# Kernel optimization log

Hardware: AMD Instinct MI355X
Metric: run time of the kernel (lower is better)

## Reference

```python
import jax, jax.numpy as jnp
import numpy as np
from jax import lax

B, T, F_IN = 8, 512, 229
C1 = 48            # model_size_conv // 16
C3 = 96            # model_size_conv // 8
D_CONV = 768       # model_size_conv
D_LSTM = 768       # model_size_lstm
N_PITCH = 88       # MAX_MIDI - MIN_MIDI + 1
N_STATE = 5
EMB = 2
LSTM_IN = D_CONV + N_PITCH * EMB   # 944
FC_IN = C3 * (F_IN // 4)           # 96 * 57 = 5472
BN_EPS = 1e-5


def setup_inputs() -> dict:
    key = jax.random.key(0)
    ks = iter(jax.random.split(key, 64))
    nrm = lambda shape, s=0.05: jax.random.normal(next(ks), shape, jnp.float32) * s
    uni = lambda shape: jax.random.uniform(next(ks), shape, jnp.float32, 0.5, 1.5)
    inp = {
        'mel': jax.random.normal(next(ks), (B, T, F_IN), jnp.float32),
        'conv1_w': nrm((C1, 1, 3, 3)), 'conv1_b': nrm((C1,)),
        'bn1_g': uni((C1,)), 'bn1_b': nrm((C1,)), 'bn1_m': nrm((C1,), 0.1), 'bn1_v': uni((C1,)),
        'conv2_w': nrm((C1, C1, 3, 3)), 'conv2_b': nrm((C1,)),
        'bn2_g': uni((C1,)), 'bn2_b': nrm((C1,)), 'bn2_m': nrm((C1,), 0.1), 'bn2_v': uni((C1,)),
        'conv3_w': nrm((C3, C1, 3, 3)), 'conv3_b': nrm((C3,)),
        'bn3_g': uni((C3,)), 'bn3_b': nrm((C3,)), 'bn3_m': nrm((C3,), 0.1), 'bn3_v': uni((C3,)),
        'fc_w': nrm((D_CONV, FC_IN)), 'fc_b': nrm((D_CONV,)),
        'wih1': nrm((4 * D_LSTM, LSTM_IN)), 'whh1': nrm((4 * D_LSTM, D_LSTM)),
        'bih1': nrm((4 * D_LSTM,)), 'bhh1': nrm((4 * D_LSTM,)),
        'wih2': nrm((4 * D_LSTM, D_LSTM)), 'whh2': nrm((4 * D_LSTM, D_LSTM)),
        'bih2': nrm((4 * D_LSTM,)), 'bhh2': nrm((4 * D_LSTM,)),
        'post_w': nrm((N_PITCH * N_STATE, D_LSTM)), 'post_b': nrm((N_PITCH * N_STATE,)),
        'emb_w': nrm((N_STATE, EMB), 1.0),
    }
    return inp


def _conv_bn_relu(x, w, b, g, be, m, v):
    # x: NCHW, w: OIHW, padding 'SAME' == padding=1 for 3x3
    y = lax.conv_general_dilated(x, w, (1, 1), 'SAME', dimension_numbers=('NCHW', 'OIHW', 'NCHW'))
    y = y + b[None, :, None, None]
    scale = (g / jnp.sqrt(v + BN_EPS))[None, :, None, None]
    y = (y - m[None, :, None, None]) * scale + be[None, :, None, None]
    return jax.nn.relu(y)


def _maxpool12(x):
    # MaxPool2d((1,2)) on NCHW, floor mode
    return lax.reduce_window(x, -jnp.inf, lax.max, (1, 1, 1, 2), (1, 1, 1, 2), 'VALID')


def _lstm_cell(x, h, c, wih, whh, bih, bhh):
    z = x @ wih.T + h @ whh.T + bih + bhh
    i, f, g, o = jnp.split(z, 4, axis=-1)
    c = jax.nn.sigmoid(f) * c + jax.nn.sigmoid(i) * jnp.tanh(g)
    h = jax.nn.sigmoid(o) * jnp.tanh(c)
    return h, c


def _forward(mel, conv1_w, conv1_b, bn1_g, bn1_b, bn1_m, bn1_v,
             conv2_w, conv2_b, bn2_g, bn2_b, bn2_m, bn2_v,
             conv3_w, conv3_b, bn3_g, bn3_b, bn3_m, bn3_v,
             fc_w, fc_b, wih1, whh1, bih1, bhh1, wih2, whh2, bih2, bhh2,
             post_w, post_b, emb_w):
    b = mel.shape[0]
    # --- ConvStack acoustic model (eval mode: dropout = identity) ---
    x = mel[:, None]                                  # (B,1,T,F)
    x = _conv_bn_relu(x, conv1_w, conv1_b, bn1_g, bn1_b, bn1_m, bn1_v)
    x = _conv_bn_relu(x, conv2_w, conv2_b, bn2_g, bn2_b, bn2_m, bn2_v)
    x = _maxpool12(x)
    x = _conv_bn_relu(x, conv3_w, conv3_b, bn3_g, bn3_b, bn3_m, bn3_v)
    x = _maxpool12(x)                                 # (B,C3,T,F//4)
    x = x.transpose(0, 2, 1, 3).reshape(b, -1, FC_IN) # (B,T,C3*F//4)
    acoustic = x @ fc_w.T + fc_b                      # (B,T,768)

    def step(carry, a_t):
        h1, c1, h2, c2, prev = carry                  # prev: (B,88) int32
        emb = emb_w[prev].reshape(prev.shape[0], N_PITCH * EMB)
        xt = jnp.concatenate([a_t, emb], axis=-1)     # (B,944)
        h1n, c1n = _lstm_cell(xt, h1, c1, wih1, whh1, bih1, bhh1)
        h2n, c2n = _lstm_cell(h1n, h2, c2, wih2, whh2, bih2, bhh2)
        logits = (h2n @ post_w.T + post_b).reshape(-1, N_PITCH, N_STATE)
        nprev = jnp.argmax(logits, axis=-1).astype(jnp.int32)  # argmax(softmax)==argmax(logits)
        return (h1n, c1n, h2n, c2n, nprev), logits

    z = jnp.zeros((b, D_LSTM), mel.dtype)
    prev0 = jnp.zeros((b, N_PITCH), jnp.int32)
    _, logits = lax.scan(step, (z, z, z, z, prev0), acoustic.transpose(1, 0, 2))
    return logits.transpose(1, 0, 2, 3)               # (B,T,88,N_STATE)


def reference(mel, conv1_w, conv1_b, bn1_g, bn1_b, bn1_m, bn1_v,
              conv2_w, conv2_b, bn2_g, bn2_b, bn2_m, bn2_v,
              conv3_w, conv3_b, bn3_g, bn3_b, bn3_m, bn3_v,
              fc_w, fc_b, wih1, whh1, bih1, bhh1, wih2, whh2, bih2, bhh2,
              post_w, post_b, emb_w):
    return _forward(mel, conv1_w, conv1_b, bn1_g, bn1_b, bn1_m, bn1_v,
                    conv2_w, conv2_b, bn2_g, bn2_b, bn2_m, bn2_v,
                    conv3_w, conv3_b, bn3_g, bn3_b, bn3_m, bn3_v,
                    fc_w, fc_b, wih1, whh1, bih1, bhh1, wih2, whh2, bih2, bhh2,
                    post_w, post_b, emb_w)
```

## Files before the change

### kernel.cpp

```cpp
#include <hip/hip_runtime.h>
#include <math.h>

#define WS_C3   0u
#define WS_C2CH 22413312u
#define WS_AC   28104192u
#define WS_A1   0u
#define WS_ST   31249920u

__device__ __forceinline__ float sigm(float x){ return 1.0f / (1.0f + expf(-x)); }

__device__ __forceinline__ void cstore(float* p, float v){
  union { float f; unsigned u; } c; c.f = v;
  __hip_atomic_store((unsigned*)p, c.u, __ATOMIC_RELAXED,
                     __HIP_MEMORY_SCOPE_SYSTEM);
}
__device__ __forceinline__ void cload64(const float* p, float& a, float& b){
  unsigned long long u = __hip_atomic_load((const unsigned long long*)p,
                          __ATOMIC_RELAXED, __HIP_MEMORY_SCOPE_SYSTEM);
  union { unsigned long long u; float f[2]; } c; c.u = u;
  a = c.f[0]; b = c.f[1];
}
__device__ __forceinline__ unsigned cloadu(const unsigned* p){
  return __hip_atomic_load(p, __ATOMIC_RELAXED, __HIP_MEMORY_SCOPE_SYSTEM);
}

#define SLOT 16
#define FLG  4112
__device__ __forceinline__ void gbar(unsigned* sy, unsigned bar, int wg){
  __syncthreads();
  const int tid = threadIdx.x;
  if (tid == 0)
    __hip_atomic_store(&sy[SLOT + wg*16], bar, __ATOMIC_RELAXED,
                       __HIP_MEMORY_SCOPE_SYSTEM);
  if (wg == 255){
    if (tid < 64){
      for (;;){
        unsigned m0 = cloadu(&sy[SLOT + (4*tid + 0)*16]);
        unsigned m1 = cloadu(&sy[SLOT + (4*tid + 1)*16]);
        unsigned m2 = cloadu(&sy[SLOT + (4*tid + 2)*16]);
        unsigned m3 = cloadu(&sy[SLOT + (4*tid + 3)*16]);
        unsigned a = m0 < m1 ? m0 : m1;
        unsigned b = m2 < m3 ? m2 : m3;
        unsigned mn = a < b ? a : b;
        if (__all(mn >= bar)) break;
        __builtin_amdgcn_s_sleep(1);
      }
    }
    __syncthreads();
    __hip_atomic_store(&sy[FLG + tid*16], bar, __ATOMIC_RELAXED,
                       __HIP_MEMORY_SCOPE_SYSTEM);
  } else {
    if (tid == 0){
      while (cloadu(&sy[FLG + wg*16]) < bar)
        __builtin_amdgcn_s_sleep(1);
    }
  }
  __syncthreads();
}

__global__ __launch_bounds__(256) void conv2f_k(
    const float* __restrict__ mel, const float* __restrict__ w1,
    const float* __restrict__ b1, const float* __restrict__ g1,
    const float* __restrict__ be1, const float* __restrict__ m1,
    const float* __restrict__ v1,
    const float* __restrict__ w2, const float* __restrict__ b2,
    const float* __restrict__ g2, const float* __restrict__ be2,
    const float* __restrict__ m2, const float* __restrict__ v2,
    float* __restrict__ c2ch, int t0)
{
  __shared__ float act[3*8*240];
  __shared__ float w2s[48*8*12];
  __shared__ float mel5[5*240];
  __shared__ float w1s[48*12];
  __shared__ float sc1[48], sh1[48], sc2[48], sh2[48];
  int tid = threadIdx.x;
  int b = blockIdx.x / 130, lt = blockIdx.x - b*130;
  int t = t0 - 1 + lt;

  int fg = tid % 29, ocg = tid / 29;
  int f0 = fg * 8, oc0 = ocg * 6;

  if (t < 0 || t > 511){
    if (tid < 232){
      for (int o = 0; o < 6; ++o)
        for (int jj = 0; jj < 4; ++jj){
          int fp = fg*4 + jj;
          if (fp < 114)
            c2ch[((b*48 + oc0 + o)*130 + lt)*114 + fp] = 0.f;
        }
    }
    return;
  }

  for (int idx = tid; idx < 5*240; idx += 256){
    int rr = idx / 240, w = idx - rr*240;
    int tt = t + rr - 2, f = w - 2;
    mel5[idx] = (tt >= 0 && tt < 512 && f >= 0 && f < 229)
                ? mel[(b*512 + tt)*229 + f] : 0.f;
  }
  for (int idx = tid; idx < 48*12; idx += 256){
    int c = idx / 12, q = idx - c*12;
    int kh = q >> 2, kw = q & 3;
    w1s[idx] = (kw < 3) ? w1[c*9 + kh*3 + kw] : 0.f;
  }
  if (tid < 48){
    float s1 = g1[tid] / sqrtf(v1[tid] + 1e-5f);
    sc1[tid] = s1; sh1[tid] = be1[tid] + (b1[tid] - m1[tid]) * s1;
    float s2 = g2[tid] / sqrtf(v2[tid] + 1e-5f);
    sc2[tid] = s2; sh2[tid] = be2[tid] + (b2[tid] - m2[tid]) * s2;
  }

  float acc[6][8];
  #pragma unroll
  for (int o = 0; o < 6; ++o)
    #pragma unroll
    for (int j = 0; j < 8; ++j) acc[o][j] = 0.f;

  for (int ch = 0; ch < 6; ++ch){
    int ci0 = ch * 8;
    __syncthreads();
    for (int idx = tid; idx < 3*8*240; idx += 256){
      int rr = idx / 1920;
      int rem = idx - rr*1920;
      int ci = rem / 240, w = rem - ci*240;
      int tt = t + rr - 1, f = w - 1;
      float val = 0.f;
      if (tt >= 0 && tt < 512 && f >= 0 && f < 229){
        int cg = ci0 + ci;
        float a = 0.f;
        #pragma unroll
        for (int dh = 0; dh < 3; ++dh){
          const float* mr = &mel5[(rr + dh)*240 + w];
          a = fmaf(mr[0], w1s[cg*12 + dh*4 + 0], a);
          a = fmaf(mr[1], w1s[cg*12 + dh*4 + 1], a);
          a = fmaf(mr[2], w1s[cg*12 + dh*4 + 2], a);
        }
        a = a * sc1[cg] + sh1[cg];
        val = a > 0.f ? a : 0.f;
      }
      act[idx] = val;
    }
    for (int idx = tid; idx < 48*8*12; idx += 256){
      int oc = idx / 96;
      int rem = idx - oc*96;
      int ci = rem / 12, q = rem - ci*12;
      int kh = q >> 2, kw = q & 3;
      w2s[idx] = (kw < 3) ? w2[(oc*48 + ci0 + ci)*9 + kh*3 + kw] : 0.f;
    }
    __syncthreads();
    if (tid < 232){
      for (int ci = 0; ci < 8; ++ci){
        #pragma unroll
        for (int kh = 0; kh < 3; ++kh){
          const float* ap = &act[(kh*8 + ci)*240 + f0];
          float4 A0 = *(const float4*)(ap);
          float4 A1v = *(const float4*)(ap + 4);
          float4 A2 = *(const float4*)(ap + 8);
          float L[12] = {A0.x,A0.y,A0.z,A0.w,A1v.x,A1v.y,A1v.z,A1v.w,A2.x,A2.y,A2.z,A2.w};
          #pragma unroll
          for (int o = 0; o < 6; ++o){
            float4 wv = *(const float4*)&w2s[((oc0 + o)*8 + ci)*12 + kh*4];
            #pragma unroll
            for (int j = 0; j < 8; ++j)
              acc[o][j] = fmaf(L[j+2], wv.z, fmaf(L[j+1], wv.y, fmaf(L[j], wv.x, acc[o][j])));
          }
        }
      }
    }
  }
  __syncthreads();
  if (tid < 232){
    #pragma unroll
    for (int o = 0; o < 6; ++o){
      int oc = oc0 + o;
      float s = sc2[oc], hs = sh2[oc];
      #pragma unroll
      for (int jj = 0; jj < 4; ++jj){
        int fp = fg*4 + jj;
        if (fp < 114){
          float v0 = acc[o][2*jj] * s + hs;   v0 = v0 > 0.f ? v0 : 0.f;
          float v1 = acc[o][2*jj+1] * s + hs; v1 = v1 > 0.f ? v1 : 0.f;
          c2ch[((b*48 + oc)*130 + lt)*114 + fp] = v0 > v1 ? v0 : v1;
        }
      }
    }
  }
}

__global__ __launch_bounds__(256) void conv3_k(
    const float* __restrict__ c2ch, const float* __restrict__ w3,
    const float* __restrict__ b3, const float* __restrict__ g3,
    const float* __restrict__ be3, const float* __restrict__ m3,
    const float* __restrict__ v3, float* __restrict__ c3p, int t0)
{
  __shared__ float act[3*8*128];
  __shared__ float w3s[96*8*12];
  __shared__ float sc[96], sh[96];
  int tid = threadIdx.x;
  int b = blockIdx.x >> 7, tl = blockIdx.x & 127;
  int t = t0 + tl;
  if (tid < 96){
    float s = g3[tid] / sqrtf(v3[tid] + 1e-5f);
    sc[tid] = s; sh[tid] = be3[tid] + (b3[tid] - m3[tid]) * s;
  }
  int fg = tid % 15, ocg = tid / 15;
  int f0 = fg * 8, oc0 = ocg * 6;
  float acc[6][8];
  #pragma unroll
  for (int o = 0; o < 6; ++o)
    #pragma unroll
    for (int j = 0; j < 8; ++j) acc[o][j] = 0.f;

  for (int ch = 0; ch < 6; ++ch){
    int ci0 = ch * 8;
    __syncthreads();
    for (int idx = tid; idx < 3*8*128; idx += 256){
      int rr = idx >> 10;
      int rem = idx & 1023;
      int ci = rem >> 7, w = rem & 127;
      int lt = tl + rr;
      int f = w - 1;
      float val = 0.f;
      if (f >= 0 && f < 114)
        val = c2ch[((b*48 + ci0 + ci)*130 + lt)*114 + f];
      act[idx] = val;
    }
    for (int idx = tid; idx < 96*8*12; idx += 256){
      int oc = idx / 96;
      int rem = idx - oc*96;
      int ci = rem / 12, q = rem - ci*12;
      int kh = q >> 2, kw = q & 3;
      w3s[idx] = (kw < 3) ? w3[(oc*48 + ci0 + ci)*9 + kh*3 + kw] : 0.f;
    }
    __syncthreads();
    if (tid < 240){
      for (int ci = 0; ci < 8; ++ci){
        #pragma unroll
        for (int kh = 0; kh < 3; ++kh){
          const float* ap = &act[(kh*8 + ci)*128 + f0];
          float4 A0 = *(const float4*)(ap);
          float4 A1v = *(const float4*)(ap + 4);
          float4 A2 = *(const float4*)(ap + 8);
          float L[12] = {A0.x,A0.y,A0.z,A0.w,A1v.x,A1v.y,A1v.z,A1v.w,A2.x,A2.y,A2.z,A2.w};
          #pragma unroll
          for (int o = 0; o < 6; ++o){
            float4 wv = *(const float4*)&w3s[((oc0 + o)*8 + ci)*12 + kh*4];
            #pragma unroll
            for (int j = 0; j < 8; ++j)
              acc[o][j] = fmaf(L[j+2], wv.z, fmaf(L[j+1], wv.y, fmaf(L[j], wv.x, acc[o][j])));
          }
        }
      }
    }
  }
  __syncthreads();
  if (tid < 240){
    #pragma unroll
    for (int o = 0; o < 6; ++o){
      int oc = oc0 + o;
      float s = sc[oc], hs = sh[oc];
      #pragma unroll
      for (int jj = 0; jj < 4; ++jj){
        int fp = fg*4 + jj;
        if (fp < 57){
          float v0 = acc[o][2*jj] * s + hs;   v0 = v0 > 0.f ? v0 : 0.f;
          float v1 = acc[o][2*jj+1] * s + hs; v1 = v1 > 0.f ? v1 : 0.f;
          c3p[((b*96 + oc)*512 + t)*57 + fp] = v0 > v1 ? v0 : v1;
        }
      }
    }
  }
}

__global__ __launch_bounds__(256) void gemm_fc_k(
    const float* __restrict__ c3p, const float* __restrict__ fcw,
    const float* __restrict__ fcb, float* __restrict__ ac)
{
  __shared__ float As[16*132];
  __shared__ float Bs[16*132];
  int tid = threadIdx.x;
  int m0 = blockIdx.x * 128, n0 = blockIdx.y * 128;
  int tm = (tid & 15) * 8, tn = (tid >> 4) * 8;
  float acc[8][8];
  #pragma unroll
  for (int i = 0; i < 8; ++i)
    #pragma unroll
    for (int j = 0; j < 8; ++j) acc[i][j] = 0.f;

  for (int k0 = 0; k0 < 5472; k0 += 16){
    __syncthreads();
    #pragma unroll
    for (int i = 0; i < 8; ++i){
      int idx = i*256 + tid;
      int k = idx & 15, mm = idx >> 4;
      int gk = k0 + k;
      int ci = (gk * 36793) >> 21;
      int f  = gk - ci*57;
      int gm = m0 + mm;
      int bb = gm >> 9, tt = gm & 511;
      As[k*132 + mm] = c3p[((bb*96 + ci)*512 + tt)*57 + f];
      Bs[k*132 + mm] = fcw[(n0 + mm)*5472 + gk];
    }
    __syncthreads();
    #pragma unroll
    for (int k = 0; k < 16; ++k){
      const float* arow = &As[k*132 + tm];
      const float* brow = &Bs[k*132 + tn];
      float4 a0 = *(const float4*)arow, a1 = *(const float4*)(arow + 4);
      float4 b0 = *(const float4*)brow, b1 = *(const float4*)(brow + 4);
      float av[8] = {a0.x,a0.y,a0.z,a0.w,a1.x,a1.y,a1.z,a1.w};
      float bv[8] = {b0.x,b0.y,b0.z,b0.w,b1.x,b1.y,b1.z,b1.w};
      #pragma unroll
      for (int i = 0; i < 8; ++i)
        #pragma unroll
        for (int j = 0; j < 8; ++j)
          acc[i][j] = fmaf(av[i], bv[j], acc[i][j]);
    }
  }
  #pragma unroll
  for (int i = 0; i < 8; ++i){
    int gm = m0 + tm + i;
    #pragma unroll
    for (int j = 0; j < 8; ++j){
      int gn = n0 + tn + j;
      ac[gm*768 + gn] = acc[i][j] + fcb[gn];
    }
  }
}

__global__ __launch_bounds__(256) void gemm_a1_k(
    const float* __restrict__ ac, const float* __restrict__ wih1,
    const float* __restrict__ bih1, const float* __restrict__ bhh1,
    float* __restrict__ A1)
{
  __shared__ float As[16*132];
  __shared__ float Bs[16*132];
  int tid = threadIdx.x;
  int m0 = blockIdx.x * 128, n0 = blockIdx.y * 128;
  int tm = (tid & 15) * 8, tn = (tid >> 4) * 8;
  float acc[8][8];
  #pragma unroll
  for (int i = 0; i < 8; ++i)
    #pragma unroll
    for (int j = 0; j < 8; ++j) acc[i][j] = 0.f;

  for (int k0 = 0; k0 < 768; k0 += 16){
    __syncthreads();
    #pragma unroll
    for (int i = 0; i < 8; ++i){
      int idx = i*256 + tid;
      int k = idx & 15, mm = idx >> 4;
      int gk = k0 + k;
      As[k*132 + mm] = ac[(m0 + mm)*768 + gk];
      Bs[k*132 + mm] = wih1[(n0 + mm)*944 + gk];
    }
    __syncthreads();
    #pragma unroll
    for (int k = 0; k < 16; ++k){
      const float* arow = &As[k*132 + tm];
      const float* brow = &Bs[k*132 + tn];
      float4 a0 = *(const float4*)arow, a1 = *(const float4*)(arow + 4);
      float4 b0 = *(const float4*)brow, b1 = *(const float4*)(brow + 4);
      float av[8] = {a0.x,a0.y,a0.z,a0.w,a1.x,a1.y,a1.z,a1.w};
      float bv[8] = {b0.x,b0.y,b0.z,b0.w,b1.x,b1.y,b1.z,b1.w};
      #pragma unroll
      for (int i = 0; i < 8; ++i)
        #pragma unroll
        for (int j = 0; j < 8; ++j)
          acc[i][j] = fmaf(av[i], bv[j], acc[i][j]);
    }
  }
  #pragma unroll
  for (int i = 0; i < 8; ++i){
    int gm = m0 + tm + i;
    int tt = gm & 511, bb = gm >> 9;
    #pragma unroll
    for (int j = 0; j < 8; ++j){
      int gn = n0 + tn + j;
      A1[tt*24576 + gn*8 + bb] = acc[i][j] + bih1[gn] + bhh1[gn];
    }
  }
}

#define SA 948
#define S2 772
__global__ __launch_bounds__(256, 1) void rec_k(
    const float* __restrict__ A1,
    const float* __restrict__ whh1, const float* __restrict__ wih1,
    const float* __restrict__ wih2, const float* __restrict__ whh2,
    const float* __restrict__ bih2, const float* __restrict__ bhh2,
    const float* __restrict__ postw, const float* __restrict__ postb,
    const float* __restrict__ embw,
    float* __restrict__ xbuf, float* __restrict__ h2b,
    unsigned* __restrict__ sy, float* __restrict__ out)
{
  const int wg = blockIdx.x, tid = threadIdx.x;
  const int wv = tid >> 6, l = tid & 63;
  __shared__ float xs[8*SA];
  __shared__ float h2s[8*S2];
  __shared__ float zbuf[96];
  __shared__ float red2[160];

  float wA[15][3];
  float wB[24][3];
  float wC[3][5];
  {
    int Rb = wv*768 + wg*3;
    #pragma unroll
    for (int ki = 0; ki < 15; ++ki){
      int k = l + (ki << 6);
      #pragma unroll
      for (int u = 0; u < 3; ++u){
        float w = 0.f;
        if (k < 768) w = whh1[(Rb + u)*768 + k];
        else if (k < 944) w = wih1[(Rb + u)*944 + k];
        wA[ki][u] = w;
      }
    }
    #pragma unroll
    for (int ki = 0; ki < 24; ++ki){
      int k = l + (ki << 6);
      #pragma unroll
      for (int u = 0; u < 3; ++u)
        wB[ki][u] = (k < 768) ? wih2[(Rb + u)*768 + k] : whh2[(Rb + u)*768 + k - 768];
    }
  }
  if (wg < 88){
    #pragma unroll
    for (int kc = 0; kc < 3; ++kc)
      #pragma unroll
      for (int s = 0; s < 5; ++s)
        wC[kc][s] = postw[(wg*5 + s)*768 + tid + (kc << 8)];
  }
  float b2r = 0.f; int fR = 0, fb = 0;
  if (tid < 96){
    int g = tid / 24, rem = tid - g*24;
    int u = rem >> 3; fb = rem & 7;
    fR = g*768 + wg*3 + u;
    b2r = bih2[fR] + bhh2[fR];
  }
  float pbr = (wg < 88 && tid < 40) ? postb[wg*5 + (tid >> 3)] : 0.f;
  float c1r = 0.f, c2r = 0.f;

  for (int idx = tid; idx < 8*S2; idx += 256) h2s[idx] = 0.f;
  if (wg == 0){
    for (int idx = tid; idx < 1408; idx += 256){
      int e = idx >> 3, bb = idx & 7;
      cstore(&xbuf[(768 + e)*8 + bb], embw[e & 1]);
    }
  }
  unsigned bar = 1;
  gbar(sy, bar, wg);

  for (int t = 0; t < 512; ++t){
    const int cur = t & 1, nxt = cur ^ 1;
    float* xc  = xbuf + cur * 7552;
    float* xn  = xbuf + nxt * 7552;
    float* h2n = h2b + nxt * 6144;

    float a1v = 0.f;
    if (tid < 96) a1v = A1[t*24576 + fR*8 + fb];

    {
      for (int idx = tid; idx < 3776; idx += 256){
        float a, b; cload64(xc + 2*idx, a, b);
        int k = idx >> 2, p = (idx & 3) << 1;
        xs[p*SA + k]       = a;
        xs[(p + 1)*SA + k] = b;
      }
      __syncthreads();
      float acc[3][8];
      #pragma unroll
      for (int u = 0; u < 3; ++u)
        #pragma unroll
        for (int j = 0; j < 8; ++j) acc[u][j] = 0.f;
      #pragma unroll
      for (int ki = 0; ki < 15; ++ki){
        int k = l + (ki << 6);
        if (k < 944){
          float x0 = xs[k],        x1 = xs[SA + k],   x2 = xs[2*SA + k], x3 = xs[3*SA + k];
          float x4 = xs[4*SA + k], x5 = xs[5*SA + k], x6 = xs[6*SA + k], x7 = xs[7*SA + k];
          #pragma unroll
          for (int u = 0; u < 3; ++u){
            float w = wA[ki][u];
            acc[u][0] = fmaf(w, x0, acc[u][0]);
            acc[u][1] = fmaf(w, x1, acc[u][1]);
            acc[u][2] = fmaf(w, x2, acc[u][2]);
            acc[u][3] = fmaf(w, x3, acc[u][3]);
            acc[u][4] = fmaf(w, x4, acc[u][4]);
            acc[u][5] = fmaf(w, x5, acc[u][5]);
            acc[u][6] = fmaf(w, x6, acc[u][6]);
            acc[u][7] = fmaf(w, x7, acc[u][7]);
          }
        }
      }
      #pragma unroll
      for (int u = 0; u < 3; ++u)
        #pragma unroll
        for (int j = 0; j < 8; ++j){
          float s = acc[u][j];
          s += __shfl_xor(s, 1);  s += __shfl_xor(s, 2);  s += __shfl_xor(s, 4);
          s += __shfl_xor(s, 8);  s += __shfl_xor(s, 16); s += __shfl_xor(s, 32);
          if (l == 0) zbuf[wv*24 + u*8 + j] = s;
        }
      __syncthreads();
      if (tid < 96)
        zbuf[tid] += a1v;
      __syncthreads();
      if (tid < 24){
        float zi = zbuf[tid], zf = zbuf[24 + tid], zg = zbuf[48 + tid], zo = zbuf[72 + tid];
        c1r = sigm(zf)*c1r + sigm(zi)*tanhf(zg);
        float hh = sigm(zo)*tanhf(c1r);
        cstore(&xn[(wg*3 + (tid >> 3))*8 + (tid & 7)], hh);
      }
      ++bar; gbar(sy, bar, wg);
    }

    {
      for (int idx = tid; idx < 3072; idx += 256){
        float a, b; cload64(xn + 2*idx, a, b);
        int k = idx >> 2, p = (idx & 3) << 1;
        xs[p*S2 + k]       = a;
        xs[(p + 1)*S2 + k] = b;
      }
      __syncthreads();
      float acc[3][8];
      #pragma unroll
      for (int u = 0; u < 3; ++u)
        #pragma unroll
        for (int j = 0; j < 8; ++j) acc[u][j] = 0.f;
      #pragma unroll
      for (int ki = 0; ki < 24; ++ki){
        float x0, x1, x2, x3, x4, x5, x6, x7;
        if (ki < 12){
          int k = l + (ki << 6);
          x0 = xs[k];        x1 = xs[S2 + k];   x2 = xs[2*S2 + k]; x3 = xs[3*S2 + k];
          x4 = xs[4*S2 + k]; x5 = xs[5*S2 + k]; x6 = xs[6*S2 + k]; x7 = xs[7*S2 + k];
        } else {
          int k = l + ((ki - 12) << 6);
          x0 = h2s[k];        x1 = h2s[S2 + k];   x2 = h2s[2*S2 + k]; x3 = h2s[3*S2 + k];
          x4 = h2s[4*S2 + k]; x5 = h2s[5*S2 + k]; x6 = h2s[6*S2 + k]; x7 = h2s[7*S2 + k];
        }
        #pragma unroll
        for (int u = 0; u < 3; ++u){
          float w = wB[ki][u];
          acc[u][0] = fmaf(w, x0, acc[u][0]);
          acc[u][1] = fmaf(w, x1, acc[u][1]);
          acc[u][2] = fmaf(w, x2, acc[u][2]);
          acc[u][3] = fmaf(w, x3, acc[u][3]);
          acc[u][4] = fmaf(w, x4, acc[u][4]);
          acc[u][5] = fmaf(w, x5, acc[u][5]);
          acc[u][6] = fmaf(w, x6, acc[u][6]);
          acc[u][7] = fmaf(w, x7, acc[u][7]);
        }
      }
      #pragma unroll
      for (int u = 0; u < 3; ++u)
        #pragma unroll
        for (int j = 0; j < 8; ++j){
          float s = acc[u][j];
          s += __shfl_xor(s, 1);  s += __shfl_xor(s, 2);  s += __shfl_xor(s, 4);
          s += __shfl_xor(s, 8);  s += __shfl_xor(s, 16); s += __shfl_xor(s, 32);
          if (l == 0) zbuf[wv*24 + u*8 + j] = s;
        }
      __syncthreads();
      if (tid < 96)
        zbuf[tid] += b2r;
      __syncthreads();
      if (tid < 24){
        float zi = zbuf[tid], zf = zbuf[24 + tid], zg = zbuf[48 + tid], zo = zbuf[72 + tid];
        c2r = sigm(zf)*c2r + sigm(zi)*tanhf(zg);
        float hh = sigm(zo)*tanhf(c2r);
        cstore(&h2n[(wg*3 + (tid >> 3))*8 + (tid & 7)], hh);
      }
      ++bar; gbar(sy, bar, wg);
    }

    {
      for (int idx = tid; idx < 3072; idx += 256){
        float a, b; cload64(h2n + 2*idx, a, b);
        int k = idx >> 2, p = (idx & 3) << 1;
        h2s[p*S2 + k]       = a;
        h2s[(p + 1)*S2 + k] = b;
      }
      __syncthreads();
      if (wg < 88){
        float acc[5][8];
        #pragma unroll
        for (int s = 0; s < 5; ++s)
          #pragma unroll
          for (int j = 0; j < 8; ++j) acc[s][j] = 0.f;
        #pragma unroll
        for (int kc = 0; kc < 3; ++kc){
          int k = tid + (kc << 8);
          float x0 = h2s[k],        x1 = h2s[S2 + k],   x2 = h2s[2*S2 + k], x3 = h2s[3*S2 + k];
          float x4 = h2s[4*S2 + k], x5 = h2s[5*S2 + k], x6 = h2s[6*S2 + k], x7 = h2s[7*S2 + k];
          #pragma unroll
          for (int s = 0; s < 5; ++s){
            float w = wC[kc][s];
            acc[s][0] = fmaf(w, x0, acc[s][0]);
            acc[s][1] = fmaf(w, x1, acc[s][1]);
            acc[s][2] = fmaf(w, x2, acc[s][2]);
            acc[s][3] = fmaf(w, x3, acc[s][3]);
            acc[s][4] = fmaf(w, x4, acc[s][4]);
            acc[s][5] = fmaf(w, x5, acc[s][5]);
            acc[s][6] = fmaf(w, x6, acc[s][6]);
            acc[s][7] = fmaf(w, x7, acc[s][7]);
          }
        }
        #pragma unroll
        for (int s = 0; s < 5; ++s)
          #pragma unroll
          for (int j = 0; j < 8; ++j){
            float v = acc[s][j];
            v += __shfl_xor(v, 1);  v += __shfl_xor(v, 2);  v += __shfl_xor(v, 4);
            v += __shfl_xor(v, 8);  v += __shfl_xor(v, 16); v += __shfl_xor(v, 32);
            if (l == 0) red2[(s*8 + j)*4 + wv] = v;
          }
        __syncthreads();
        if (tid < 40){
          float sum = red2[tid*4] + red2[tid*4 + 1] + red2[tid*4 + 2] + red2[tid*4 + 3] + pbr;
          int s = tid >> 3, bb = tid & 7;
          out[bb*225280 + t*440 + wg*5 + s] = sum;
          zbuf[tid] = sum;
        }
        __syncthreads();
        if (tid < 8){
          float best = zbuf[tid]; int bs = 0;
          #pragma unroll
          for (int s = 1; s < 5; ++s){
            float v = zbuf[s*8 + tid];
            if (v > best){ best = v; bs = s; }
          }
          cstore(&xn[(768 + wg*2)*8 + tid],     embw[bs*2]);
          cstore(&xn[(768 + wg*2 + 1)*8 + tid], embw[bs*2 + 1]);
        }
      }
      ++bar; gbar(sy, bar, wg);
    }
  }
}

extern "C" void kernel_launch(void* const* d_in, const int* in_sizes, int n_in,
                              void* d_out, int out_size, void* d_ws, size_t ws_size,
                              hipStream_t stream)
{
  (void)in_sizes; (void)n_in; (void)out_size; (void)ws_size;
  const float* mel  = (const float*)d_in[0];
  const float* w1   = (const float*)d_in[1];
  const float* b1   = (const float*)d_in[2];
  const float* g1   = (const float*)d_in[3];
  const float* be1  = (const float*)d_in[4];
  const float* m1   = (const float*)d_in[5];
  const float* v1   = (const float*)d_in[6];
  const float* w2   = (const float*)d_in[7];
  const float* b2   = (const float*)d_in[8];
  const float* g2   = (const float*)d_in[9];
  const float* be2  = (const float*)d_in[10];
  const float* m2   = (const float*)d_in[11];
  const float* v2   = (const float*)d_in[12];
  const float* w3   = (const float*)d_in[13];
  const float* b3   = (const float*)d_in[14];
  const float* g3   = (const float*)d_in[15];
  const float* be3  = (const float*)d_in[16];
  const float* m3   = (const float*)d_in[17];
  const float* v3   = (const float*)d_in[18];
  const float* fcw  = (const float*)d_in[19];
  const float* fcb  = (const float*)d_in[20];
  const float* wih1 = (const float*)d_in[21];
  const float* whh1 = (const float*)d_in[22];
  const float* bih1 = (const float*)d_in[23];
  const float* bhh1 = (const float*)d_in[24];
  const float* wih2 = (const float*)d_in[25];
  const float* whh2 = (const float*)d_in[26];
  const float* bih2 = (const float*)d_in[27];
  const float* bhh2 = (const float*)d_in[28];
  const float* postw= (const float*)d_in[29];
  const float* postb= (const float*)d_in[30];
  const float* embw = (const float*)d_in[31];

  float* ws    = (float*)d_ws;
  float* c3p   = ws + WS_C3;
  float* c2ch  = ws + WS_C2CH;
  float* ac    = ws + WS_AC;
  float* A1    = ws + WS_A1;
  float* st    = ws + WS_ST;
  float* xbuf  = st;
  float* h2b   = st + 15104;
  unsigned* sy = (unsigned*)(st + 27392);
  float* outp  = (float*)d_out;

  hipMemsetAsync(st, 0, 35600 * sizeof(float), stream);

  for (int c = 0; c < 4; ++c){
    int t0 = c * 128;
    conv2f_k<<<dim3(8*130), dim3(256), 0, stream>>>(
        mel, w1, b1, g1, be1, m1, v1, w2, b2, g2, be2, m2, v2, c2ch, t0);
    conv3_k<<<dim3(8*128), dim3(256), 0, stream>>>(
        c2ch, w3, b3, g3, be3, m3, v3, c3p, t0);
  }
  gemm_fc_k<<<dim3(32, 6), dim3(256), 0, stream>>>(c3p, fcw, fcb, ac);
  gemm_a1_k<<<dim3(32, 24), dim3(256), 0, stream>>>(ac, wih1, bih1, bhh1, A1);

  rec_k<<<dim3(256), dim3(256), 0, stream>>>(
      A1, whh1, wih1, wih2, whh2, bih2, bhh2, postw, postb, embw,
      xbuf, h2b, sy, outp);
}
```

Measured before the change: 22.25 ms.

## Replace embedding-feedback grid barrier with per-pitch flag slots and precomputed embedding contributions

The pitch-state embedding input to LSTM1 is no longer written to global memory and reduced through a full grid barrier. Each output workgroup publishes its packed argmax states with a timestep tag in a 64-bit slot. Every workgroup polls these slots and adds precomputed wih1·embedding contributions from a shared-memory table. This removes one grid-wide barrier per timestep and shrinks the LSTM1 dot product to the 768 recurrent inputs. It also reorders LSTM2 so the h2 part is computed while the fresh h1 loads are in flight, and keeps the post-projection inputs in registers. The cost is spin-polling on 88 slots and a serial 88-iteration gather per gate row.

After: 19.00 ms. -14.6%, faster.

```diff
diff --git a/kernel.cpp b/kernel.cpp
--- a/kernel.cpp
+++ b/kernel.cpp
@@ -23,9 +23,18 @@
 __device__ __forceinline__ unsigned cloadu(const unsigned* p){
   return __hip_atomic_load(p, __ATOMIC_RELAXED, __HIP_MEMORY_SCOPE_SYSTEM);
 }
+__device__ __forceinline__ unsigned long long cloadu64(const void* p){
+  return __hip_atomic_load((const unsigned long long*)p, __ATOMIC_RELAXED,
+                           __HIP_MEMORY_SCOPE_SYSTEM);
+}
+__device__ __forceinline__ void cstoreu64(void* p, unsigned long long v){
+  __hip_atomic_store((unsigned long long*)p, v, __ATOMIC_RELAXED,
+                     __HIP_MEMORY_SCOPE_SYSTEM);
+}
 
 #define SLOT 16
 #define FLG  4112
+#define SLOTX 8208
 __device__ __forceinline__ void gbar(unsigned* sy, unsigned bar, int wg){
   __syncthreads();
   const int tid = threadIdx.x;
@@ -382,7 +391,6 @@
   }
 }
 
-#define SA 948
 #define S2 772
 __global__ __launch_bounds__(256, 1) void rec_k(
     const float* __restrict__ A1,
@@ -396,26 +404,24 @@
 {
   const int wg = blockIdx.x, tid = threadIdx.x;
   const int wv = tid >> 6, l = tid & 63;
-  __shared__ float xs[8*SA];
+  __shared__ float xs[8*S2];
   __shared__ float h2s[8*S2];
+  __shared__ float cvec[88*5*12];
   __shared__ float zbuf[96];
   __shared__ float red2[160];
-
-  float wA[15][3];
+  __shared__ unsigned smax[88];
+
+  float wA[12][3];
   float wB[24][3];
   float wC[3][5];
   {
     int Rb = wv*768 + wg*3;
     #pragma unroll
-    for (int ki = 0; ki < 15; ++ki){
+    for (int ki = 0; ki < 12; ++ki){
       int k = l + (ki << 6);
       #pragma unroll
-      for (int u = 0; u < 3; ++u){
-        float w = 0.f;
-        if (k < 768) w = whh1[(Rb + u)*768 + k];
-        else if (k < 944) w = wih1[(Rb + u)*944 + k];
-        wA[ki][u] = w;
-      }
+      for (int u = 0; u < 3; ++u)
+        wA[ki][u] = whh1[(Rb + u)*768 + k];
     }
     #pragma unroll
     for (int ki = 0; ki < 24; ++ki){
@@ -442,19 +448,21 @@
   float pbr = (wg < 88 && tid < 40) ? postb[wg*5 + (tid >> 3)] : 0.f;
   float c1r = 0.f, c2r = 0.f;
 
-  for (int idx = tid; idx < 8*S2; idx += 256) h2s[idx] = 0.f;
-  if (wg == 0){
-    for (int idx = tid; idx < 1408; idx += 256){
-      int e = idx >> 3, bb = idx & 7;
-      cstore(&xbuf[(768 + e)*8 + bb], embw[e & 1]);
-    }
-  }
-  unsigned bar = 1;
-  gbar(sy, bar, wg);
+  for (int idx = tid; idx < 88*5*12; idx += 256){
+    int p = idx / 60, rem = idx - p*60;
+    int s = rem / 12, r = rem - s*12;
+    int g = r / 3, u = r - g*3;
+    int row = g*768 + wg*3 + u;
+    cvec[idx] = wih1[row*944 + 768 + 2*p]     * embw[s*2]
+              + wih1[row*944 + 768 + 2*p + 1] * embw[s*2 + 1];
+  }
+  for (int idx = tid; idx < 8*S2; idx += 256){ h2s[idx] = 0.f; xs[idx] = 0.f; }
+  __syncthreads();
+
+  unsigned bar = 0;
 
   for (int t = 0; t < 512; ++t){
-    const int cur = t & 1, nxt = cur ^ 1;
-    float* xc  = xbuf + cur * 7552;
+    const int nxt = (t & 1) ^ 1;
     float* xn  = xbuf + nxt * 7552;
     float* h2n = h2b + nxt * 6144;
 
@@ -462,38 +470,30 @@
     if (tid < 96) a1v = A1[t*24576 + fR*8 + fb];
 
     {
-      for (int idx = tid; idx < 3776; idx += 256){
-        float a, b; cload64(xc + 2*idx, a, b);
-        int k = idx >> 2, p = (idx & 3) << 1;
-        xs[p*SA + k]       = a;
-        xs[(p + 1)*SA + k] = b;
+      float acc[3][8];
+      #pragma unroll
+      for (int u = 0; u < 3; ++u)
+        #pragma unroll
+        for (int j = 0; j < 8; ++j) acc[u][j] = 0.f;
+      #pragma unroll
+      for (int ki = 0; ki < 12; ++ki){
+        int k = l + (ki << 6);
+        float x0 = xs[k],        x1 = xs[S2 + k],   x2 = xs[2*S2 + k], x3 = xs[3*S2 + k];
+        float x4 = xs[4*S2 + k], x5 = xs[5*S2 + k], x6 = xs[6*S2 + k], x7 = xs[7*S2 + k];
+        #pragma unroll
+        for (int u = 0; u < 3; ++u){
+          float w = wA[ki][u];
+          acc[u][0] = fmaf(w, x0, acc[u][0]);
+          acc[u][1] = fmaf(w, x1, acc[u][1]);
+          acc[u][2] = fmaf(w, x2, acc[u][2]);
+          acc[u][3] = fmaf(w, x3, acc[u][3]);
+          acc[u][4] = fmaf(w, x4, acc[u][4]);
+          acc[u][5] = fmaf(w, x5, acc[u][5]);
+          acc[u][6] = fmaf(w, x6, acc[u][6]);
+          acc[u][7] = fmaf(w, x7, acc[u][7]);
+        }
       }
       __syncthreads();
-      float acc[3][8];
-      #pragma unroll
-      for (int u = 0; u < 3; ++u)
-        #pragma unroll
-        for (int j = 0; j < 8; ++j) acc[u][j] = 0.f;
-      #pragma unroll
-      for (int ki = 0; ki < 15; ++ki){
-        int k = l + (ki << 6);
-        if (k < 944){
-          float x0 = xs[k],        x1 = xs[SA + k],   x2 = xs[2*SA + k], x3 = xs[3*SA + k];
-          float x4 = xs[4*SA + k], x5 = xs[5*SA + k], x6 = xs[6*SA + k], x7 = xs[7*SA + k];
-          #pragma unroll
-          for (int u = 0; u < 3; ++u){
-            float w = wA[ki][u];
-            acc[u][0] = fmaf(w, x0, acc[u][0]);
-            acc[u][1] = fmaf(w, x1, acc[u][1]);
-            acc[u][2] = fmaf(w, x2, acc[u][2]);
-            acc[u][3] = fmaf(w, x3, acc[u][3]);
-            acc[u][4] = fmaf(w, x4, acc[u][4]);
-            acc[u][5] = fmaf(w, x5, acc[u][5]);
-            acc[u][6] = fmaf(w, x6, acc[u][6]);
-            acc[u][7] = fmaf(w, x7, acc[u][7]);
-          }
-        }
-      }
       #pragma unroll
       for (int u = 0; u < 3; ++u)
         #pragma unroll
@@ -503,9 +503,34 @@
           s += __shfl_xor(s, 8);  s += __shfl_xor(s, 16); s += __shfl_xor(s, 32);
           if (l == 0) zbuf[wv*24 + u*8 + j] = s;
         }
+      if (wv == 0){
+        unsigned long long* sl = (unsigned long long*)&sy[SLOTX];
+        unsigned lo0 = 0, lo1 = 0;
+        for (;;){
+          unsigned long long v0 = cloadu64(&sl[l*8]);
+          unsigned long long v1 = 0xffffffffffffffffull;
+          if (l < 24) v1 = cloadu64(&sl[(64 + l)*8]);
+          unsigned t0v = (unsigned)(v0 >> 32);
+          unsigned t1v = (unsigned)(v1 >> 32);
+          unsigned mn = t0v < t1v ? t0v : t1v;
+          if (__all(mn >= (unsigned)t)){ lo0 = (unsigned)v0; lo1 = (unsigned)v1; break; }
+          __builtin_amdgcn_s_sleep(1);
+        }
+        smax[l] = lo0;
+        if (l < 24) smax[64 + l] = lo1;
+      }
       __syncthreads();
-      if (tid < 96)
-        zbuf[tid] += a1v;
+      if (tid < 96){
+        int g = tid / 24;
+        int rowidx = g*3 + ((tid - g*24) >> 3);
+        int b = tid & 7;
+        float z = zbuf[tid] + a1v;
+        for (int p = 0; p < 88; ++p){
+          int s = (smax[p] >> (b*4)) & 7;
+          z += cvec[(p*5 + s)*12 + rowidx];
+        }
+        zbuf[tid] = z;
+      }
       __syncthreads();
       if (tid < 24){
         float zi = zbuf[tid], zf = zbuf[24 + tid], zg = zbuf[48 + tid], zo = zbuf[72 + tid];
@@ -517,30 +542,22 @@
     }
 
     {
-      for (int idx = tid; idx < 3072; idx += 256){
-        float a, b; cload64(xn + 2*idx, a, b);
-        int k = idx >> 2, p = (idx & 3) << 1;
-        xs[p*S2 + k]       = a;
-        xs[(p + 1)*S2 + k] = b;
-      }
-      __syncthreads();
+      float sa[12], sb[12];
+      #pragma unroll
+      for (int i = 0; i < 12; ++i){
+        int idx = tid + (i << 8);
+        cload64(xn + 2*idx, sa[i], sb[i]);
+      }
       float acc[3][8];
       #pragma unroll
       for (int u = 0; u < 3; ++u)
         #pragma unroll
         for (int j = 0; j < 8; ++j) acc[u][j] = 0.f;
       #pragma unroll
-      for (int ki = 0; ki < 24; ++ki){
-        float x0, x1, x2, x3, x4, x5, x6, x7;
-        if (ki < 12){
-          int k = l + (ki << 6);
-          x0 = xs[k];        x1 = xs[S2 + k];   x2 = xs[2*S2 + k]; x3 = xs[3*S2 + k];
-          x4 = xs[4*S2 + k]; x5 = xs[5*S2 + k]; x6 = xs[6*S2 + k]; x7 = xs[7*S2 + k];
-        } else {
-          int k = l + ((ki - 12) << 6);
-          x0 = h2s[k];        x1 = h2s[S2 + k];   x2 = h2s[2*S2 + k]; x3 = h2s[3*S2 + k];
-          x4 = h2s[4*S2 + k]; x5 = h2s[5*S2 + k]; x6 = h2s[6*S2 + k]; x7 = h2s[7*S2 + k];
-        }
+      for (int ki = 12; ki < 24; ++ki){
+        int k = l + ((ki - 12) << 6);
+        float x0 = h2s[k],        x1 = h2s[S2 + k],   x2 = h2s[2*S2 + k], x3 = h2s[3*S2 + k];
+        float x4 = h2s[4*S2 + k], x5 = h2s[5*S2 + k], x6 = h2s[6*S2 + k], x7 = h2s[7*S2 + k];
         #pragma unroll
         for (int u = 0; u < 3; ++u){
           float w = wB[ki][u];
@@ -555,6 +572,32 @@
         }
       }
       #pragma unroll
+      for (int i = 0; i < 12; ++i){
+        int idx = tid + (i << 8);
+        int k = idx >> 2, p = (idx & 3) << 1;
+        xs[p*S2 + k]       = sa[i];
+        xs[(p + 1)*S2 + k] = sb[i];
+      }
+      __syncthreads();
+      #pragma unroll
+      for (int ki = 0; ki < 12; ++ki){
+        int k = l + (ki << 6);
+        float x0 = xs[k],        x1 = xs[S2 + k],   x2 = xs[2*S2 + k], x3 = xs[3*S2 + k];
+        float x4 = xs[4*S2 + k], x5 = xs[5*S2 + k], x6 = xs[6*S2 + k], x7 = xs[7*S2 + k];
+        #pragma unroll
+        for (int u = 0; u < 3; ++u){
+          float w = wB[ki][u];
+          acc[u][0] = fmaf(w, x0, acc[u][0]);
+          acc[u][1] = fmaf(w, x1, acc[u][1]);
+          acc[u][2] = fmaf(w, x2, acc[u][2]);
+          acc[u][3] = fmaf(w, x3, acc[u][3]);
+          acc[u][4] = fmaf(w, x4, acc[u][4]);
+          acc[u][5] = fmaf(w, x5, acc[u][5]);
+          acc[u][6] = fmaf(w, x6, acc[u][6]);
+          acc[u][7] = fmaf(w, x7, acc[u][7]);
+        }
+      }
+      #pragma unroll
       for (int u = 0; u < 3; ++u)
         #pragma unroll
         for (int j = 0; j < 8; ++j){
@@ -577,37 +620,27 @@
     }
 
     {
-      for (int idx = tid; idx < 3072; idx += 256){
-        float a, b; cload64(h2n + 2*idx, a, b);
-        int k = idx >> 2, p = (idx & 3) << 1;
-        h2s[p*S2 + k]       = a;
-        h2s[(p + 1)*S2 + k] = b;
-      }
-      __syncthreads();
+      float r0[8], r1[8], r2[8];
+      #pragma unroll
+      for (int q = 0; q < 4; ++q){
+        cload64(h2n + (tid        )*8 + 2*q, r0[2*q], r0[2*q+1]);
+        cload64(h2n + (tid + 256  )*8 + 2*q, r1[2*q], r1[2*q+1]);
+        cload64(h2n + (tid + 512  )*8 + 2*q, r2[2*q], r2[2*q+1]);
+      }
+      #pragma unroll
+      for (int p = 0; p < 8; ++p){
+        h2s[p*S2 + tid]       = r0[p];
+        h2s[p*S2 + tid + 256] = r1[p];
+        h2s[p*S2 + tid + 512] = r2[p];
+      }
       if (wg < 88){
         float acc[5][8];
         #pragma unroll
         for (int s = 0; s < 5; ++s)
           #pragma unroll
-          for (int j = 0; j < 8; ++j) acc[s][j] = 0.f;
-        #pragma unroll
-        for (int kc = 0; kc < 3; ++kc){
-          int k = tid + (kc << 8);
-          float x0 = h2s[k],        x1 = h2s[S2 + k],   x2 = h2s[2*S2 + k], x3 = h2s[3*S2 + k];
-          float x4 = h2s[4*S2 + k], x5 = h2s[5*S2 + k], x6 = h2s[6*S2 + k], x7 = h2s[7*S2 + k];
-          #pragma unroll
-          for (int s = 0; s < 5; ++s){
-            float w = wC[kc][s];
-            acc[s][0] = fmaf(w, x0, acc[s][0]);
-            acc[s][1] = fmaf(w, x1, acc[s][1]);
-            acc[s][2] = fmaf(w, x2, acc[s][2]);
-            acc[s][3] = fmaf(w, x3, acc[s][3]);
-            acc[s][4] = fmaf(w, x4, acc[s][4]);
-            acc[s][5] = fmaf(w, x5, acc[s][5]);
-            acc[s][6] = fmaf(w, x6, acc[s][6]);
-            acc[s][7] = fmaf(w, x7, acc[s][7]);
-          }
-        }
+          for (int j = 0; j < 8; ++j)
+            acc[s][j] = fmaf(wC[2][s], r2[j],
+                        fmaf(wC[1][s], r1[j], wC[0][s]*r0[j]));
         #pragma unroll
         for (int s = 0; s < 5; ++s)
           #pragma unroll
@@ -625,18 +658,27 @@
           zbuf[tid] = sum;
         }
         __syncthreads();
+        int bs = 0;
         if (tid < 8){
-          float best = zbuf[tid]; int bs = 0;
+          float best = zbuf[tid];
           #pragma unroll
           for (int s = 1; s < 5; ++s){
             float v = zbuf[s*8 + tid];
             if (v > best){ best = v; bs = s; }
           }
-          cstore(&xn[(768 + wg*2)*8 + tid],     embw[bs*2]);
-          cstore(&xn[(768 + wg*2 + 1)*8 + tid], embw[bs*2 + 1]);
-        }
-      }
-      ++bar; gbar(sy, bar, wg);
+        }
+        if (wv == 0){
+          unsigned lo = 0;
+          #pragma unroll
+          for (int b = 0; b < 8; ++b)
+            lo |= (unsigned)(__shfl(bs, b) & 7) << (4*b);
+          if (l == 0){
+            unsigned long long pv =
+                ((unsigned long long)(unsigned)(t + 1) << 32) | (unsigned long long)lo;
+            cstoreu64(&sy[SLOTX + wg*16], pv);
+          }
+        }
+      }
     }
   }
 }
@@ -690,7 +732,7 @@
   unsigned* sy = (unsigned*)(st + 27392);
   float* outp  = (float*)d_out;
 
-  hipMemsetAsync(st, 0, 35600 * sizeof(float), stream);
+  hipMemsetAsync(st, 0, 37008 * sizeof(float), stream);
 
   for (int c = 0; c < 4; ++c){
     int t0 = c * 128;
```
